# Kernel optimization log

Measured on AMD Instinct MI355X. Metric: run time of the kernel, lower is better.

The kernel has to match this reference:

```python
import jax, jax.numpy as jnp
import numpy as np

_CODESZ = 8
_IDX_OFFSET = -2 ** 15


def _build_grid_part():
    # Truncated codebook: unique |grid| rows. abs of base {-3.5..2.5} is {0.5,1.5,2.5,3.5};
    # every such combo with ||v||^2 <= 10 is realizable, and np.meshgrid(ij) cartesian
    # product of ascending values yields lexicographically sorted rows, matching
    # torch.unique(torch.abs(grid), dim=0).
    vals = np.arange(4, dtype=np.float32) + 0.5
    grid = np.stack(np.meshgrid(*([vals] * _CODESZ), indexing='ij'), axis=-1).reshape(-1, _CODESZ)
    gn = (grid ** 2).sum(-1)
    keep = gn <= 10
    return grid[keep], gn[keep]  # [227, 8], [227]


def setup_inputs() -> dict:
    key = jax.random.key(0)
    X = jax.random.normal(key, (1048576, _CODESZ), dtype=jnp.float32)
    gp, gpn = _build_grid_part()
    int_map = jnp.asarray(2 ** np.arange(_CODESZ), dtype=jnp.int32)  # [8]
    return {
        'X': X,
        'grid_part': jnp.asarray(gp),
        'grid_part_norm': jnp.asarray(gpn),
        'int_map': int_map,
    }


def reference(X, grid_part, grid_part_norm, int_map):
    neg = X < 0  # [N, 8] bool
    # sign bit-pack: sum_i 2^i * neg_i, shifted into high byte
    flips = jnp.sum(int_map * neg.astype(jnp.int32), axis=-1) << 8  # [N]
    mask = 1.0 - 2.0 * neg.astype(X.dtype)  # +/-1
    X_part = jnp.abs(X)
    # nearest-codeword search: argmax of 2<x,g> - ||g||^2
    scores = 2.0 * jnp.einsum('nc,gc->ng', X_part, grid_part) - grid_part_norm  # [N, 227]
    Xqidx = jnp.argmax(scores, axis=-1)  # [N]
    vals = grid_part[Xqidx] * mask  # [N, 8]
    idxs = (flips + Xqidx.astype(jnp.int32) + _IDX_OFFSET).astype(jnp.int16)  # [N]
    return vals, idxs
```

## Files before the change

kernel.cpp:

```cpp
#include <hip/hip_runtime.h>


constexpr int CODESZ = 8;
constexpr int NGRID  = 227;
constexpr int NKEYS  = 6561;

constexpr unsigned GT_ONE = 0x3F800008u;

__global__ __launch_bounds__(256, 8)
void hi2b_kernel(const float* __restrict__ X,
                 const float* __restrict__ grid_part,
                 float* __restrict__ out_vals,
                 float* __restrict__ out_idxs,
                 int n_rows, int rows_per_block)
{
    __shared__ unsigned short s_lut[NKEYS];
    const int t = threadIdx.x;

    if (t < NGRID) {
        const float4* gp4 = reinterpret_cast<const float4*>(grid_part);
        const float4 ga = gp4[t * 2];
        const float4 gb = gp4[t * 2 + 1];
        const int key = (int)ga.x       + (int)ga.y * 3   + (int)ga.z * 9
                      + (int)ga.w * 27  + (int)gb.x * 81  + (int)gb.y * 243
                      + (int)gb.z * 729 + (int)gb.w * 2187;
        s_lut[key] = (unsigned short)t;
    }
    __syncthreads();

    const int base = blockIdx.x * rows_per_block;

    for (int r0 = 0; r0 < rows_per_block; r0 += 256) {
        const int row = base + r0 + t;
        if (row >= n_rows) continue;

        const float4* xp = reinterpret_cast<const float4*>(X + (size_t)row * CODESZ);
        const float4 va = xp[0];
        const float4 vb = xp[1];

        unsigned pk[8];
        int flips = 0;
        {
            const float xx[8] = {va.x, va.y, va.z, va.w, vb.x, vb.y, vb.z, vb.w};
#pragma unroll
            for (int i = 0; i < 8; ++i) {
                const unsigned b = __float_as_uint(xx[i]);
                flips |= (int)(b >> 31) << i;
                pk[i] = ((b & 0x7FFFFFF8u)) | (unsigned)i;
            }
        }

        unsigned s0 = pk[0], s1 = pk[1], s2 = pk[2], s3 = pk[3];
        unsigned s4 = pk[4], s5 = pk[5], s6 = pk[6], s7 = pk[7];
#define CASD(a, b) { const unsigned _hi = (a) > (b) ? (a) : (b); const unsigned _lo = (a) > (b) ? (b) : (a); (a) = _hi; (b) = _lo; }
        CASD(s0, s1) CASD(s2, s3) CASD(s4, s5) CASD(s6, s7)
        CASD(s0, s2) CASD(s1, s3) CASD(s4, s6) CASD(s5, s7)
        CASD(s1, s2) CASD(s5, s6) CASD(s0, s4) CASD(s3, s7)
        CASD(s1, s5) CASD(s2, s6)
        CASD(s1, s4) CASD(s3, s6)
        CASD(s2, s4) CASD(s3, s5)
        CASD(s3, s4)
#undef CASD

        const float y1 = __uint_as_float(s0 & 0xFFFFFFF8u);
        const float y2 = __uint_as_float(s1 & 0xFFFFFFF8u);
        const float y3 = __uint_as_float(s2 & 0xFFFFFFF8u);
        const float y4 = __uint_as_float(s3 & 0xFFFFFFF8u);
        const float t1 = fmaxf(y1 - 1.0f, 0.0f);
        const float t2 = fmaxf(y2 - 1.0f, 0.0f);
        const float t3 = fmaxf(y3 - 1.0f, 0.0f);
        const float t4 = fmaxf(y4 - 1.0f, 0.0f);
        const float Ap = (t1 + t2) + (t3 + t4);
        const float Bp = 2.0f * y1 - 3.0f + t2;
        const bool useB = Bp > Ap;

        const unsigned tA   = (s3 > GT_ONE) ? s3 : GT_ONE;
        const bool     b1ok = (s1 >= GT_ONE);

        int key = 0;
        float ov[8];
#pragma unroll
        for (int i = 0; i < 8; ++i) {
            constexpr int P3[8] = {1, 3, 9, 27, 81, 243, 729, 2187};
            const int dA = (pk[i] >= tA) ? 1 : 0;
            const int dB = (pk[i] == s0) ? 2 : ((b1ok && pk[i] == s1) ? 1 : 0);
            const int d  = useB ? dB : dA;
            key += d * P3[i];
            const float v = 0.5f + (float)d;
            ov[i] = ((flips >> i) & 1) ? -v : v;
        }

        const int rank = s_lut[key];

        float4* op = reinterpret_cast<float4*>(out_vals + (size_t)row * CODESZ);
        op[0] = make_float4(ov[0], ov[1], ov[2], ov[3]);
        op[1] = make_float4(ov[4], ov[5], ov[6], ov[7]);
        out_idxs[row] = (float)((flips << 8) + rank - 32768);
    }
}

extern "C" void kernel_launch(void* const* d_in, const int* in_sizes, int n_in,
                              void* d_out, int out_size, void* d_ws, size_t ws_size,
                              hipStream_t stream) {
    const float* X         = (const float*)d_in[0];
    const float* grid_part = (const float*)d_in[1];

    const int n_rows = in_sizes[0] / CODESZ;

    float* out_vals = (float*)d_out;
    float* out_idxs = out_vals + (size_t)n_rows * CODESZ;

    const int blocks = 2048;
    const int rows_per_block = (n_rows + blocks - 1) / blocks;

    hi2b_kernel<<<blocks, 256, 0, stream>>>(X, grid_part, out_vals, out_idxs,
                                            n_rows, rows_per_block);
}
```

Measured before the change: 17.37 us.

## Compute codeword rank combinatorially instead of via shared-memory lookup table

Replaces the per-block shared-memory LUT, which was built from grid_part and indexed by a base-3 key, with an arithmetic rank computed from a constant table of combinatorial counts (ranking multisets within the norm budget). This removes the LUT build, the __syncthreads, and the shared-memory read, and lets the launch use one row per thread over many small blocks instead of a grid-stride-style loop. The grid_part input is no longer read, so correctness now depends on the hardcoded codebook ordering matching the one built by the reference.

```diff
diff --git a/kernel.cpp b/kernel.cpp
--- a/kernel.cpp
+++ b/kernel.cpp
@@ -1,118 +1,113 @@
 #include <hip/hip_runtime.h>
 
 
+typedef float floatx4 __attribute__((ext_vector_type(4)));
+
 constexpr int CODESZ = 8;
-constexpr int NGRID  = 227;
-constexpr int NKEYS  = 6561;
 
 constexpr unsigned GT_ONE = 0x3F800008u;
 
+constexpr unsigned long long NT[8] = {
+    0x0101010101ULL,
+    0x0303020201ULL,
+    0x0806040301ULL,
+    0x110B070401ULL,
+    0x20130B0501ULL,
+    0x381F100601ULL,
+    0x5D30160701ULL,
+    0x94471D0801ULL,
+};
+
 __global__ __launch_bounds__(256, 8)
 void hi2b_kernel(const float* __restrict__ X,
-                 const float* __restrict__ grid_part,
                  float* __restrict__ out_vals,
                  float* __restrict__ out_idxs,
-                 int n_rows, int rows_per_block)
+                 int n_rows)
 {
-    __shared__ unsigned short s_lut[NKEYS];
-    const int t = threadIdx.x;
+    const int row = blockIdx.x * 256 + threadIdx.x;
+    if (row >= n_rows) return;
 
-    if (t < NGRID) {
-        const float4* gp4 = reinterpret_cast<const float4*>(grid_part);
-        const float4 ga = gp4[t * 2];
-        const float4 gb = gp4[t * 2 + 1];
-        const int key = (int)ga.x       + (int)ga.y * 3   + (int)ga.z * 9
-                      + (int)ga.w * 27  + (int)gb.x * 81  + (int)gb.y * 243
-                      + (int)gb.z * 729 + (int)gb.w * 2187;
-        s_lut[key] = (unsigned short)t;
+    const floatx4* xp = reinterpret_cast<const floatx4*>(X + (size_t)row * CODESZ);
+    const floatx4 va = xp[0];
+    const floatx4 vb = xp[1];
+
+    unsigned pk[8];
+    int flips = 0;
+    {
+        const float xx[8] = {va.x, va.y, va.z, va.w, vb.x, vb.y, vb.z, vb.w};
+#pragma unroll
+        for (int i = 0; i < 8; ++i) {
+            const unsigned b = __float_as_uint(xx[i]);
+            flips |= (int)(b >> 31) << i;
+            pk[i] = (b & 0x7FFFFFF8u) | (unsigned)i;
+        }
     }
-    __syncthreads();
 
-    const int base = blockIdx.x * rows_per_block;
-
-    for (int r0 = 0; r0 < rows_per_block; r0 += 256) {
-        const int row = base + r0 + t;
-        if (row >= n_rows) continue;
-
-        const float4* xp = reinterpret_cast<const float4*>(X + (size_t)row * CODESZ);
-        const float4 va = xp[0];
-        const float4 vb = xp[1];
-
-        unsigned pk[8];
-        int flips = 0;
-        {
-            const float xx[8] = {va.x, va.y, va.z, va.w, vb.x, vb.y, vb.z, vb.w};
-#pragma unroll
-            for (int i = 0; i < 8; ++i) {
-                const unsigned b = __float_as_uint(xx[i]);
-                flips |= (int)(b >> 31) << i;
-                pk[i] = ((b & 0x7FFFFFF8u)) | (unsigned)i;
-            }
-        }
-
-        unsigned s0 = pk[0], s1 = pk[1], s2 = pk[2], s3 = pk[3];
-        unsigned s4 = pk[4], s5 = pk[5], s6 = pk[6], s7 = pk[7];
+    unsigned s0 = pk[0], s1 = pk[1], s2 = pk[2], s3 = pk[3];
+    unsigned s4 = pk[4], s5 = pk[5], s6 = pk[6], s7 = pk[7];
 #define CASD(a, b) { const unsigned _hi = (a) > (b) ? (a) : (b); const unsigned _lo = (a) > (b) ? (b) : (a); (a) = _hi; (b) = _lo; }
-        CASD(s0, s1) CASD(s2, s3) CASD(s4, s5) CASD(s6, s7)
-        CASD(s0, s2) CASD(s1, s3) CASD(s4, s6) CASD(s5, s7)
-        CASD(s1, s2) CASD(s5, s6) CASD(s0, s4) CASD(s3, s7)
-        CASD(s1, s5) CASD(s2, s6)
-        CASD(s1, s4) CASD(s3, s6)
-        CASD(s2, s4) CASD(s3, s5)
-        CASD(s3, s4)
+    CASD(s0, s1) CASD(s2, s3) CASD(s4, s5) CASD(s6, s7)
+    CASD(s0, s2) CASD(s1, s3) CASD(s4, s6) CASD(s5, s7)
+    CASD(s1, s2) CASD(s5, s6) CASD(s0, s4) CASD(s3, s7)
+    CASD(s1, s5) CASD(s2, s6)
+    CASD(s1, s4) CASD(s3, s6)
+    CASD(s2, s4) CASD(s3, s5)
+    CASD(s3, s4)
 #undef CASD
 
-        const float y1 = __uint_as_float(s0 & 0xFFFFFFF8u);
-        const float y2 = __uint_as_float(s1 & 0xFFFFFFF8u);
-        const float y3 = __uint_as_float(s2 & 0xFFFFFFF8u);
-        const float y4 = __uint_as_float(s3 & 0xFFFFFFF8u);
-        const float t1 = fmaxf(y1 - 1.0f, 0.0f);
-        const float t2 = fmaxf(y2 - 1.0f, 0.0f);
-        const float t3 = fmaxf(y3 - 1.0f, 0.0f);
-        const float t4 = fmaxf(y4 - 1.0f, 0.0f);
-        const float Ap = (t1 + t2) + (t3 + t4);
-        const float Bp = 2.0f * y1 - 3.0f + t2;
-        const bool useB = Bp > Ap;
+    const float y1 = __uint_as_float(s0 & 0xFFFFFFF8u);
+    const float y2 = __uint_as_float(s1 & 0xFFFFFFF8u);
+    const float y3 = __uint_as_float(s2 & 0xFFFFFFF8u);
+    const float y4 = __uint_as_float(s3 & 0xFFFFFFF8u);
+    const float t1 = fmaxf(y1 - 1.0f, 0.0f);
+    const float t2 = fmaxf(y2 - 1.0f, 0.0f);
+    const float t3 = fmaxf(y3 - 1.0f, 0.0f);
+    const float t4 = fmaxf(y4 - 1.0f, 0.0f);
+    const float Ap = (t1 + t2) + (t3 + t4);
+    const float Bp = 2.0f * y1 - 3.0f + t2;
+    const bool useB = Bp > Ap;
 
-        const unsigned tA   = (s3 > GT_ONE) ? s3 : GT_ONE;
-        const bool     b1ok = (s1 >= GT_ONE);
+    const unsigned tA   = (s3 > GT_ONE) ? s3 : GT_ONE;
+    const bool     b1ok = (s1 >= GT_ONE);
 
-        int key = 0;
-        float ov[8];
+    int rank = 0;
+    int m = 4;
+    float ov[8];
 #pragma unroll
-        for (int i = 0; i < 8; ++i) {
-            constexpr int P3[8] = {1, 3, 9, 27, 81, 243, 729, 2187};
-            const int dA = (pk[i] >= tA) ? 1 : 0;
-            const int dB = (pk[i] == s0) ? 2 : ((b1ok && pk[i] == s1) ? 1 : 0);
-            const int d  = useB ? dB : dA;
-            key += d * P3[i];
-            const float v = 0.5f + (float)d;
-            ov[i] = ((flips >> i) & 1) ? -v : v;
-        }
+    for (int i = 0; i < 8; ++i) {
+        const int dA = (pk[i] >= tA) ? 1 : 0;
+        const int dB = (pk[i] == s0) ? 2 : ((b1ok && pk[i] == s1) ? 1 : 0);
+        const int d  = useB ? dB : dA;
 
-        const int rank = s_lut[key];
+        const unsigned long long Tk = NT[7 - i];
+        const int e1 = (int)((unsigned)(Tk >> (m * 8)) & 0xFFu);
+        const int e2 = (int)((unsigned)(Tk >> ((m * 8 - 8) & 63)) & 0xFFu);
+        rank += (d >= 1 ? e1 : 0) + (d == 2 ? e2 : 0);
+        m -= (d == 2) ? 3 : d;
 
-        float4* op = reinterpret_cast<float4*>(out_vals + (size_t)row * CODESZ);
-        op[0] = make_float4(ov[0], ov[1], ov[2], ov[3]);
-        op[1] = make_float4(ov[4], ov[5], ov[6], ov[7]);
-        out_idxs[row] = (float)((flips << 8) + rank - 32768);
+        const float v = 0.5f + (float)d;
+        ov[i] = ((flips >> i) & 1) ? -v : v;
     }
+
+    floatx4* op = reinterpret_cast<floatx4*>(out_vals + (size_t)row * CODESZ);
+    floatx4 w0; w0.x = ov[0]; w0.y = ov[1]; w0.z = ov[2]; w0.w = ov[3];
+    floatx4 w1; w1.x = ov[4]; w1.y = ov[5]; w1.z = ov[6]; w1.w = ov[7];
+    op[0] = w0;
+    op[1] = w1;
+    out_idxs[row] = (float)((flips << 8) + rank - 32768);
 }
 
 extern "C" void kernel_launch(void* const* d_in, const int* in_sizes, int n_in,
                               void* d_out, int out_size, void* d_ws, size_t ws_size,
                               hipStream_t stream) {
-    const float* X         = (const float*)d_in[0];
-    const float* grid_part = (const float*)d_in[1];
+    const float* X = (const float*)d_in[0];
 
     const int n_rows = in_sizes[0] / CODESZ;
 
     float* out_vals = (float*)d_out;
     float* out_idxs = out_vals + (size_t)n_rows * CODESZ;
 
-    const int blocks = 2048;
-    const int rows_per_block = (n_rows + blocks - 1) / blocks;
+    const int blocks = (n_rows + 255) / 256;
 
-    hi2b_kernel<<<blocks, 256, 0, stream>>>(X, grid_part, out_vals, out_idxs,
-                                            n_rows, rows_per_block);
+    hi2b_kernel<<<blocks, 256, 0, stream>>>(X, out_vals, out_idxs, n_rows);
 }
```

Result: slower. 17.98 us (+3.5%).
